# Kernel optimization log

Hardware: AMD Instinct MI355X
Metric: run time of the kernel (lower is better)

The kernel has to match this reference:

```python
import jax, jax.numpy as jnp
import numpy as np

B, DIM, W0, H0 = 4, 256, 128, 128
HEADS, HEAD_DIM = 8, 32
FOLD, PROP = 2, 4
EPS_GN = 1e-5


def _l2norm(x):
    n = jnp.linalg.norm(x, axis=-1, keepdims=True)
    return x / jnp.maximum(n, 1e-12)  # matches F.normalize eps


def _fold(t, f):
    # (b, c, f*w, f*h) -> (b*f*f, c, w, h), matching einops '(b f1 f2)' ordering
    b, c, W, H = t.shape
    w, h = W // f, H // f
    return t.reshape(b, c, f, w, f, h).transpose(0, 2, 4, 1, 3, 5).reshape(b * f * f, c, w, h)


def _unfold(t, f, b0):
    bf, c, w, h = t.shape
    return t.reshape(b0, f, f, c, w, h).transpose(0, 3, 1, 4, 2, 5).reshape(b0, c, f * w, f * h)


def _pool(t, p):
    # AdaptiveAvgPool2d((p, p)) for divisible sizes
    b, c, w, h = t.shape
    return t.reshape(b, c, p, w // p, p, h // p).mean(axis=(3, 5))


def setup_inputs() -> dict:
    key = jax.random.key(0)
    ks = jax.random.split(key, 6)
    D = HEADS * HEAD_DIM
    return {
        "x": jax.random.normal(ks[0], (B, DIM, W0, H0), jnp.float32),
        "xyz": jax.random.normal(ks[1], (B, 3, W0, H0), jnp.float32),
        "Wv": jax.random.normal(ks[2], (D, DIM, 7, 7), jnp.float32) * 0.02,
        "bv": jnp.zeros((D,), jnp.float32),
        "Wproj": jax.random.normal(ks[3], (DIM, D), jnp.float32) * 0.02,
        "bproj": jnp.zeros((DIM,), jnp.float32),
        "gn_w": jnp.ones((D,), jnp.float32),
        "gn_b": jnp.zeros((D,), jnp.float32),
        "sim_alpha": jnp.ones((1,), jnp.float32),
        "sim_beta": jnp.zeros((1,), jnp.float32),
    }


def reference(x, xyz, Wv, bv, Wproj, bproj, gn_w, gn_b, sim_alpha, sim_beta):
    # value = self.v(x): 7x7 conv, padding 3
    value = jax.lax.conv_general_dilated(
        x, Wv, (1, 1), ((3, 3), (3, 3)),
        dimension_numbers=("NCHW", "OIHW", "NCHW")) + bv[None, :, None, None]
    b0 = x.shape[0]
    # heads split: 'b (e c) w h -> (b e) c w h'
    xh = x.reshape(b0 * HEADS, HEAD_DIM, W0, H0)
    vh = value.reshape(b0 * HEADS, HEAD_DIM, W0, H0)
    xf = _fold(xh, FOLD)
    vf = _fold(vh, FOLD)
    xyzf = _fold(xyz, FOLD)
    bb, c, w, h = xf.shape
    M = PROP * PROP
    N = w * h
    centers = _pool(xf, PROP)                                   # (bb, c, p, p)
    xyz_c = _pool(xyzf, PROP)
    value_centers = _pool(vf, PROP).reshape(bb, c, M).transpose(0, 2, 1)  # (bb, M, c)
    cen = centers.reshape(bb, c, M).transpose(0, 2, 1)          # (bb, M, c)
    xpts = xf.reshape(bb, c, N).transpose(0, 2, 1)              # (bb, N, c)
    vpts = vf.reshape(bb, c, N).transpose(0, 2, 1)              # (bb, N, c)
    sim = jax.nn.sigmoid(sim_beta + sim_alpha *
                         jnp.einsum('bmc,bnc->bmn', _l2norm(cen), _l2norm(xpts)))
    bg = xyzf.shape[0]
    xyz_pts = xyzf.reshape(bg, 3, N).transpose(0, 2, 1)
    xyz_cc = xyz_c.reshape(bg, 3, M).transpose(0, 2, 1)
    sim_geo = jax.nn.sigmoid(sim_beta + sim_alpha *
                             jnp.einsum('bmc,bnc->bmn', _l2norm(xyz_cc), _l2norm(xyz_pts)))
    sim_geo = jnp.tile(sim_geo, (sim.shape[0] // sim_geo.shape[0], 1, 1))  # torch .repeat
    sim = sim * sim_geo ** 2
    # faithful mask math: scatter_(1, argmax, 1.0) into an all-ones tensor leaves it all-ones,
    # so dense_mask == 1 and split_mask == 0 exactly as in the source.
    dense_mask = jnp.ones_like(sim)
    split_mask = 1.0 - dense_mask
    denss_sim = sim * dense_mask
    split_sim = sim * split_mask
    split_out = (jnp.einsum('bmn,bnc->bmc', split_sim, vpts) + value_centers) \
                / (split_sim.sum(-1, keepdims=True) + 1.0)
    denss_out = (jnp.einsum('bmn,bnc->bmc', denss_sim, xpts) + cen) \
                / (denss_sim.sum(-1, keepdims=True) + 1.0)
    denss_pts = jnp.einsum('bmc,bmn->bnc', denss_out, denss_sim)  # (bb, N, c)
    split_pts = jnp.einsum('bmc,bmn->bnc', split_out, split_sim)
    out = (denss_pts + split_pts).transpose(0, 2, 1).reshape(bb, c, w, h)
    out = _unfold(out, FOLD, b0 * HEADS)
    out = out.reshape(b0, HEADS * HEAD_DIM, W0, H0)
    # GroupNorm with 1 group: normalize over (C, H, W) per sample
    mu = out.mean(axis=(1, 2, 3), keepdims=True)
    var = ((out - mu) ** 2).mean(axis=(1, 2, 3), keepdims=True)
    out = (out - mu) / jnp.sqrt(var + EPS_GN)
    out = out * gn_w[None, :, None, None] + gn_b[None, :, None, None]
    # proj 1x1 conv + silu
    out = jnp.einsum('bchw,oc->bohw', out, Wproj) + bproj[None, :, None, None]
    return jax.nn.silu(out)
```

## Files before the change

### kernel.cpp

```cpp
#include <hip/hip_runtime.h>
#include <stdint.h>


typedef __attribute__((ext_vector_type(8))) short short8;
typedef __attribute__((ext_vector_type(4))) float floatx4;
typedef _Float16 half8 __attribute__((ext_vector_type(8)));

#define XS_STRIDE 264
#define SIM_STRIDE 264

__device__ float g_sbp[2048*2];
__device__ float g_alpha[1024];
__device__ float g_bias[1024];
__device__ unsigned short g_Wbf[65536];
__device__ float g_cenraw[128*16*32];
__device__ float g_cenhat[128*16*32];
__device__ float g_gcenhat[16*16*4];
__device__ __attribute__((aligned(16))) _Float16 g_sim[(size_t)128*4096*16];
__device__ float g_dnum[128*16*16*32];
__device__ float g_rsum[128*16*16];

static __device__ __forceinline__ unsigned short f2bu(float f) {
  unsigned u = __float_as_uint(f);
  u += 0x7fffu + ((u >> 16) & 1u);
  return (unsigned short)(u >> 16);
}
static __device__ __forceinline__ float sum16(const float* p) {
  const float4* q = (const float4*)p;
  float4 a = q[0], b = q[1], c = q[2], d = q[3];
  return (a.x+a.y+a.z+a.w) + (b.x+b.y+b.z+b.w) + (c.x+c.y+c.z+c.w) + (d.x+d.y+d.z+d.w);
}

__global__ __launch_bounds__(64) void k0_geo(const float* __restrict__ xyz) {
  __shared__ float gc[64];
  const int gti = blockIdx.x;
  const int bg = gti >> 2, f1 = (gti >> 1) & 1, f2 = gti & 1;
  const int t = threadIdx.x;
  if (t < 48) {
    const int m = t / 3, ch = t - 3*(t/3);
    const int pi = m >> 2, pj = m & 3;
    const float* p = xyz + (size_t)(bg*3+ch)*16384 + (f1*64 + pi*16)*128 + f2*64 + pj*16;
    float s = 0.f;
    #pragma unroll
    for (int r = 0; r < 16; ++r) s += sum16(p + r*128);
    gc[m*4+ch] = s * (1.f/256.f);
  }
  __syncthreads();
  if (t < 16) {
    float g0 = gc[t*4], g1 = gc[t*4+1], g2 = gc[t*4+2];
    float inv = 1.f / fmaxf(sqrtf(g0*g0+g1*g1+g2*g2), 1e-12f);
    float* o = g_gcenhat + gti*64 + t*4;
    o[0] = g0*inv; o[1] = g1*inv; o[2] = g2*inv; o[3] = 0.f;
  }
}

__global__ __launch_bounds__(128) void k1a_cen(const float* __restrict__ x) {
  __shared__ float cenL[128];
  __shared__ float invL[4];
  const int blk = blockIdx.x;
  const int bb = blk >> 2, pi = blk & 3;
  const int b = bb >> 5, e = (bb >> 2) & 7, f1 = (bb >> 1) & 1, f2 = bb & 1;
  const int tid = threadIdx.x;
  const int c = tid >> 2, pj = tid & 3;
  const int m = pi*4 + pj;
  const float* p = x + ((size_t)(b*256 + e*32 + c)*128 + f1*64 + pi*16)*128 + f2*64 + pj*16;
  float s = 0.f;
  #pragma unroll
  for (int r = 0; r < 16; ++r) s += sum16(p + r*128);
  const float raw = s * (1.f/256.f);
  cenL[pj*32 + c] = raw;
  g_cenraw[(bb*16 + m)*32 + c] = raw;
  __syncthreads();
  if (tid < 4) {
    float ss = 0.f;
    #pragma unroll
    for (int cc = 0; cc < 32; ++cc) { float v = cenL[tid*32+cc]; ss += v*v; }
    invL[tid] = 1.f / fmaxf(sqrtf(ss), 1e-12f);
  }
  __syncthreads();
  g_cenhat[(bb*16 + m)*32 + c] = raw * invL[pj];
}

__global__ __launch_bounds__(256) void k1b_sim(const float* __restrict__ x,
                                               const float* __restrict__ xyz,
                                               const float* __restrict__ salpha,
                                               const float* __restrict__ sbeta) {
  __shared__ float xs[32*XS_STRIDE];
  __shared__ _Float16 simL[16*SIM_STRIDE];
  __shared__ float cenhatL[512];
  __shared__ float gcenL[64];
  __shared__ float rsW[4*16];
  const int blk = blockIdx.x;
  const int bb = blk >> 4, ck = blk & 15;
  const int b = bb >> 5, e = (bb >> 2) & 7, f1 = (bb >> 1) & 1, f2 = bb & 1;
  const int gti = ((e & 3) << 2) | (f1 << 1) | f2;
  const int tid = threadIdx.x, lane = tid & 63, wave = tid >> 6;
  const float alpha = salpha[0], beta = sbeta[0];
  const float* xt = x + (((size_t)(b*256 + e*32))*128 + f1*64)*128 + f2*64;

  cenhatL[tid]       = g_cenhat[bb*512 + tid];
  cenhatL[tid + 256] = g_cenhat[bb*512 + tid + 256];
  if (tid < 64) gcenL[tid] = g_gcenhat[gti*64 + tid];
  {
    const int c = tid >> 3, q = tid & 7;
    const float* src = xt + (size_t)c*16384 + (ck*4)*128;
    float* dst = xs + c*XS_STRIDE;
    #pragma unroll
    for (int k = 0; k < 8; ++k) {
      const int j = q + k*8;
      const int lr = j >> 4, lc = (j & 15)*4;
      *(float4*)(dst + lr*64 + lc) = *(const float4*)(src + lr*128 + lc);
    }
  }
  const int ng = ck*256 + tid;
  const int wi = ng >> 6, hi = ng & 63;
  float g0, g1, g2;
  {
    const float* gp = xyz + (size_t)((e & 3)*3)*16384 + (f1*64 + wi)*128 + f2*64 + hi;
    g0 = gp[0]; g1 = gp[16384]; g2 = gp[32768];
    float invg = 1.f / fmaxf(sqrtf(g0*g0+g1*g1+g2*g2), 1e-12f);
    g0 *= invg; g1 *= invg; g2 *= invg;
  }
  __syncthreads();

  float xn[32]; float ss = 0.f;
  #pragma unroll
  for (int c2 = 0; c2 < 32; ++c2) { float v = xs[c2*XS_STRIDE + tid]; xn[c2] = v; ss += v*v; }
  const float invn = 1.f / fmaxf(sqrtf(ss), 1e-12f);
  _Float16 sv[16];
  #pragma unroll
  for (int m = 0; m < 16; ++m) {
    const float* chp = cenhatL + m*32;
    float d = 0.f;
    #pragma unroll
    for (int c2 = 0; c2 < 32; ++c2) d += chp[c2]*xn[c2];
    d *= invn;
    const float* gh = gcenL + m*4;
    const float dg = gh[0]*g0 + gh[1]*g1 + gh[2]*g2;
    const float s  = 1.f/(1.f + __expf(-(beta + alpha*d)));
    const float gg = 1.f/(1.f + __expf(-(beta + alpha*dg)));
    const _Float16 h = (_Float16)(s*gg*gg);
    sv[m] = h;
    simL[m*SIM_STRIDE + tid] = h;
  }
  {
    half8 p0, p1;
    #pragma unroll
    for (int m = 0; m < 8; ++m) { p0[m] = sv[m]; p1[m] = sv[8+m]; }
    _Float16* gp = g_sim + ((size_t)bb*4096 + ng)*16;
    *(half8*)gp = p0;
    *(half8*)(gp + 8) = p1;
  }
  #pragma unroll
  for (int m = 0; m < 16; ++m) {
    float v = (float)sv[m];
    #pragma unroll
    for (int off = 1; off < 64; off <<= 1) v += __shfl_xor(v, off, 64);
    if (lane == 0) rsW[wave*16 + m] = v;
  }
  __syncthreads();
  if (tid < 16) g_rsum[(bb*16 + ck)*16 + tid] = rsW[tid] + rsW[16+tid] + rsW[32+tid] + rsW[48+tid];

  #pragma unroll
  for (int t2 = 0; t2 < 2; ++t2) {
    const int task = tid + t2*256;
    const int m = task & 15, c2 = task >> 4;
    const _Float16* sp = simL + m*SIM_STRIDE;
    const float* xp = xs + c2*XS_STRIDE;
    float acc = 0.f;
    #pragma unroll 4
    for (int j = 0; j < 32; ++j) {
      const half8 sh = *(const half8*)(sp + j*8);
      const float4 xa = *(const float4*)(xp + j*8);
      const float4 xb = *(const float4*)(xp + j*8 + 4);
      acc += (float)sh[0]*xa.x + (float)sh[1]*xa.y + (float)sh[2]*xa.z + (float)sh[3]*xa.w
           + (float)sh[4]*xb.x + (float)sh[5]*xb.y + (float)sh[6]*xb.z + (float)sh[7]*xb.w;
    }
    g_dnum[(((size_t)bb*16 + ck)*16 + m)*32 + c2] = acc;
  }
}

__global__ __launch_bounds__(256) void k1d_out(float* __restrict__ outv) {
  __shared__ float denssL[512];
  __shared__ float rsL[16];
  __shared__ float sred[8];
  const int blk = blockIdx.x;
  const int bb = blk >> 4, ck = blk & 15;
  const int b = bb >> 5, e = (bb >> 2) & 7, f1 = (bb >> 1) & 1, f2 = bb & 1;
  const int tid = threadIdx.x, lane = tid & 63, wave = tid >> 6;
  if (tid < 16) {
    float r = 1.f;
    #pragma unroll
    for (int k2 = 0; k2 < 16; ++k2) r += g_rsum[(bb*16 + k2)*16 + tid];
    rsL[tid] = r;
  }
  __syncthreads();
  #pragma unroll
  for (int t2 = 0; t2 < 2; ++t2) {
    const int idx = tid + t2*256;
    const int m = idx >> 5, c = idx & 31;
    float a = g_cenraw[bb*512 + idx];
    #pragma unroll
    for (int k2 = 0; k2 < 16; ++k2) a += g_dnum[(((size_t)bb*16 + k2)*16 + m)*32 + c];
    denssL[idx] = a / rsL[m];
  }
  __syncthreads();
  const int ng = ck*256 + tid;
  const int wi = ng >> 6, hi = ng & 63;
  float sarr[16];
  {
    const _Float16* gp = g_sim + ((size_t)bb*4096 + ng)*16;
    const half8 p0 = *(const half8*)gp;
    const half8 p1 = *(const half8*)(gp + 8);
    #pragma unroll
    for (int m = 0; m < 8; ++m) { sarr[m] = (float)p0[m]; sarr[8+m] = (float)p1[m]; }
  }
  float o[32];
  #pragma unroll
  for (int c = 0; c < 32; ++c) o[c] = 0.f;
  #pragma unroll
  for (int m = 0; m < 16; ++m) {
    const float s = sarr[m];
    const float* dp = denssL + m*32;
    #pragma unroll
    for (int c = 0; c < 32; ++c) o[c] += s*dp[c];
  }
  float* ob = outv + (((size_t)(b*256 + e*32))*128 + f1*64)*128 + f2*64 + wi*128 + hi;
  float s1 = 0.f, s2 = 0.f;
  #pragma unroll
  for (int c = 0; c < 32; ++c) { const float v = o[c]; s1 += v; s2 += v*v; ob[(size_t)c*16384] = v; }
  #pragma unroll
  for (int off = 1; off < 64; off <<= 1) { s1 += __shfl_xor(s1, off, 64); s2 += __shfl_xor(s2, off, 64); }
  if (lane == 0) { sred[wave] = s1; sred[4+wave] = s2; }
  __syncthreads();
  if (tid == 0) {
    g_sbp[blk*2]   = sred[0]+sred[1]+sred[2]+sred[3];
    g_sbp[blk*2+1] = sred[4]+sred[5]+sred[6]+sred[7];
  }
}

__global__ __launch_bounds__(256) void k2_prep(const float* __restrict__ Wp,
                                               const float* __restrict__ bpr,
                                               const float* __restrict__ gnw,
                                               const float* __restrict__ gnb) {
  __shared__ float betaL[256];
  __shared__ float rr[8];
  const int b = blockIdx.x, t = threadIdx.x, lane = t & 63, wave = t >> 6;
  float s1 = g_sbp[(b*512 + t)*2]     + g_sbp[(b*512 + 256 + t)*2];
  float s2 = g_sbp[(b*512 + t)*2 + 1] + g_sbp[(b*512 + 256 + t)*2 + 1];
  #pragma unroll
  for (int off = 1; off < 64; off <<= 1) { s1 += __shfl_xor(s1, off, 64); s2 += __shfl_xor(s2, off, 64); }
  if (lane == 0) { rr[wave] = s1; rr[4+wave] = s2; }
  __syncthreads();
  const float S1 = rr[0]+rr[1]+rr[2]+rr[3];
  const float S2 = rr[4]+rr[5]+rr[6]+rr[7];
  const float inv_n = 1.f / 4194304.f;
  const float mu  = S1 * inv_n;
  const float inv = rsqrtf(fmaxf(S2*inv_n - mu*mu, 0.f) + 1e-5f);
  const float a = inv * gnw[t];
  g_alpha[b*256 + t] = a;
  betaL[t] = gnb[t] - mu * a;
  __syncthreads();
  float k = bpr[t];
  const float* wr = Wp + t*256;
  for (int c = 0; c < 256; c += 4) {
    const float4 w = *(const float4*)(wr + c);
    k += w.x*betaL[c+0] + w.y*betaL[c+1] + w.z*betaL[c+2] + w.w*betaL[c+3];
  }
  g_bias[b*256 + t] = k;
  const int base = (b*256 + t)*64;
  for (int i = 0; i < 64; i += 4) {
    const float4 w = *(const float4*)(Wp + base + i);
    g_Wbf[base+i+0] = f2bu(w.x); g_Wbf[base+i+1] = f2bu(w.y);
    g_Wbf[base+i+2] = f2bu(w.z); g_Wbf[base+i+3] = f2bu(w.w);
  }
}

__global__ __launch_bounds__(256) void k3_proj(float* __restrict__ v) {
  __shared__ unsigned short vt[64*264];
  __shared__ float alphaL[256];
  __shared__ float biasL[256];
  const int blk = blockIdx.x;
  const int b = blk >> 8;
  const int p0 = (blk & 255) * 64;
  const int tid = threadIdx.x;
  alphaL[tid] = g_alpha[b*256 + tid];
  biasL[tid]  = g_bias[b*256 + tid];
  __syncthreads();
  {
    const int oct = tid >> 5, cl = tid & 31;
    #pragma unroll
    for (int i = 0; i < 8; ++i) {
      const int c = cl + 32*i;
      const float* src = v + ((size_t)(b*256 + c))*16384 + p0 + oct*8;
      const float4 r0 = *(const float4*)(src);
      const float4 r1 = *(const float4*)(src + 4);
      const float a = alphaL[c];
      unsigned short* w = vt + (oct*8)*264 + c;
      w[0*264] = f2bu(r0.x*a); w[1*264] = f2bu(r0.y*a);
      w[2*264] = f2bu(r0.z*a); w[3*264] = f2bu(r0.w*a);
      w[4*264] = f2bu(r1.x*a); w[5*264] = f2bu(r1.y*a);
      w[6*264] = f2bu(r1.z*a); w[7*264] = f2bu(r1.w*a);
    }
  }
  __syncthreads();
  const int lane = tid & 63, wave = tid >> 6;
  const int lm = lane & 15, quad = lane >> 4;
  const int m0 = wave*64;
  floatx4 acc[4][4] = {};
  #pragma unroll
  for (int ks = 0; ks < 8; ++ks) {
    const int k0 = ks*32 + quad*8;
    short8 afr[4], bfr[4];
    #pragma unroll
    for (int mi = 0; mi < 4; ++mi)
      afr[mi] = *(const short8*)((const short*)g_Wbf + (size_t)(m0 + mi*16 + lm)*256 + k0);
    #pragma unroll
    for (int ni = 0; ni < 4; ++ni)
      bfr[ni] = *(const short8*)((const short*)vt + (ni*16 + lm)*264 + k0);
    #pragma unroll
    for (int mi = 0; mi < 4; ++mi) {
      #pragma unroll
      for (int ni = 0; ni < 4; ++ni)
        acc[mi][ni] = __builtin_amdgcn_mfma_f32_16x16x32_bf16(afr[mi], bfr[ni], acc[mi][ni], 0, 0, 0);
    }
  }
  #pragma unroll
  for (int mi = 0; mi < 4; ++mi) {
    #pragma unroll
    for (int r = 0; r < 4; ++r) {
      const int o = m0 + mi*16 + quad*4 + r;
      const float kb = biasL[o];
      #pragma unroll
      for (int ni = 0; ni < 4; ++ni) {
        float val = acc[mi][ni][r] + kb;
        val = val / (1.f + __expf(-val));
        v[((size_t)(b*256 + o))*16384 + p0 + ni*16 + lm] = val;
      }
    }
  }
}

extern "C" void kernel_launch(void* const* d_in, const int* in_sizes, int n_in,
                              void* d_out, int out_size, void* d_ws, size_t ws_size,
                              hipStream_t stream)
{
  (void)in_sizes; (void)n_in; (void)d_ws; (void)ws_size; (void)out_size;
  const float* x     = (const float*)d_in[0];
  const float* xyz   = (const float*)d_in[1];
  const float* Wproj = (const float*)d_in[4];
  const float* bproj = (const float*)d_in[5];
  const float* gnw   = (const float*)d_in[6];
  const float* gnb   = (const float*)d_in[7];
  const float* sa    = (const float*)d_in[8];
  const float* sb    = (const float*)d_in[9];
  float* out = (float*)d_out;

  hipLaunchKernelGGL(k0_geo,  dim3(16),   dim3(64),  0, stream, xyz);
  hipLaunchKernelGGL(k1a_cen, dim3(512),  dim3(128), 0, stream, x);
  hipLaunchKernelGGL(k1b_sim, dim3(2048), dim3(256), 0, stream, x, xyz, sa, sb);
  hipLaunchKernelGGL(k1d_out, dim3(2048), dim3(256), 0, stream, out);
  hipLaunchKernelGGL(k2_prep, dim3(4),    dim3(256), 0, stream, Wproj, bproj, gnw, gnb);
  hipLaunchKernelGGL(k3_proj, dim3(1024), dim3(256), 0, stream, out);
}
```

Measured before the change: 269.1 us.

## Stage pre-norm output in fp16 layout, fold GN scale into weights, split reductions

The intermediate attention output is now written as an fp16 point-major buffer instead of fp32 NCHW into the output tensor. The projection GEMM reads it directly as fp16 MFMA operands, with the GroupNorm scale folded into per-batch fp16 weights, so the LDS transpose and conversion stage is gone. The dense-center reduction moves to a new small kernel so it is no longer recomputed by every block of k1d_out. Similarity and output dot products switch to packed fp16 fdot2, and the sim kernel drops its x LDS staging in favour of direct global loads. This cuts memory traffic and redundant work but adds fp16 precision loss and one more launch.

```diff
diff --git a/kernel.cpp b/kernel.cpp
--- a/kernel.cpp
+++ b/kernel.cpp
@@ -4,31 +4,43 @@
 
 typedef __attribute__((ext_vector_type(8))) short short8;
 typedef __attribute__((ext_vector_type(4))) float floatx4;
-typedef _Float16 half8 __attribute__((ext_vector_type(8)));
-
-#define XS_STRIDE 264
-#define SIM_STRIDE 264
+typedef __fp16 fp16x2 __attribute__((ext_vector_type(2)));
+
+#define SIMS_DW 260
 
 __device__ float g_sbp[2048*2];
 __device__ float g_alpha[1024];
 __device__ float g_bias[1024];
-__device__ unsigned short g_Wbf[65536];
+__device__ __attribute__((aligned(16))) _Float16 g_Wa[4*256*256];
 __device__ float g_cenraw[128*16*32];
 __device__ float g_cenhat[128*16*32];
 __device__ float g_gcenhat[16*16*4];
 __device__ __attribute__((aligned(16))) _Float16 g_sim[(size_t)128*4096*16];
 __device__ float g_dnum[128*16*16*32];
 __device__ float g_rsum[128*16*16];
-
-static __device__ __forceinline__ unsigned short f2bu(float f) {
-  unsigned u = __float_as_uint(f);
-  u += 0x7fffu + ((u >> 16) & 1u);
-  return (unsigned short)(u >> 16);
-}
+__device__ unsigned g_dnh2[128*256];
+__device__ __attribute__((aligned(16))) _Float16 g_preout[(size_t)128*4096*32];
+
+static __device__ __forceinline__ fp16x2 as_h2(unsigned u) { return __builtin_bit_cast(fp16x2, u); }
+static __device__ __forceinline__ unsigned pk(float a, float b) {
+  return __builtin_bit_cast(unsigned, __builtin_amdgcn_cvt_pkrtz(a, b));
+}
+#if __has_builtin(__builtin_amdgcn_fdot2)
+static __device__ __forceinline__ float fdot2(fp16x2 a, fp16x2 b, float c) {
+  return __builtin_amdgcn_fdot2(a, b, c, false);
+}
+#else
+static __device__ __forceinline__ float fdot2(fp16x2 a, fp16x2 b, float c) {
+  return c + (float)a[0]*(float)b[0] + (float)a[1]*(float)b[1];
+}
+#endif
 static __device__ __forceinline__ float sum16(const float* p) {
   const float4* q = (const float4*)p;
   float4 a = q[0], b = q[1], c = q[2], d = q[3];
   return (a.x+a.y+a.z+a.w) + (b.x+b.y+b.z+b.w) + (c.x+c.y+c.z+c.w) + (d.x+d.y+d.z+d.w);
+}
+static __device__ __forceinline__ float sigm(float z) {
+  return __builtin_amdgcn_rcpf(1.f + __expf(-z));
 }
 
 __global__ __launch_bounds__(64) void k0_geo(const float* __restrict__ xyz) {
@@ -81,15 +93,14 @@
   g_cenhat[(bb*16 + m)*32 + c] = raw * invL[pj];
 }
 
-__global__ __launch_bounds__(256) void k1b_sim(const float* __restrict__ x,
-                                               const float* __restrict__ xyz,
-                                               const float* __restrict__ salpha,
-                                               const float* __restrict__ sbeta) {
-  __shared__ float xs[32*XS_STRIDE];
-  __shared__ _Float16 simL[16*SIM_STRIDE];
-  __shared__ float cenhatL[512];
+__global__ __launch_bounds__(256, 4) void k1b_sim(const float* __restrict__ x,
+                                                  const float* __restrict__ xyz,
+                                                  const float* __restrict__ salpha,
+                                                  const float* __restrict__ sbeta) {
+  __shared__ float simS[16*SIMS_DW];
+  __shared__ unsigned chP[256];
   __shared__ float gcenL[64];
-  __shared__ float rsW[4*16];
+  __shared__ float rsW[64];
   const int blk = blockIdx.x;
   const int bb = blk >> 4, ck = blk & 15;
   const int b = bb >> 5, e = (bb >> 2) & 7, f1 = (bb >> 1) & 1, f2 = bb & 1;
@@ -98,62 +109,58 @@
   const float alpha = salpha[0], beta = sbeta[0];
   const float* xt = x + (((size_t)(b*256 + e*32))*128 + f1*64)*128 + f2*64;
 
-  cenhatL[tid]       = g_cenhat[bb*512 + tid];
-  cenhatL[tid + 256] = g_cenhat[bb*512 + tid + 256];
+  {
+    const float2 cp = *(const float2*)(g_cenhat + bb*512 + tid*2);
+    chP[tid] = pk(cp.x, cp.y);
+  }
   if (tid < 64) gcenL[tid] = g_gcenhat[gti*64 + tid];
-  {
-    const int c = tid >> 3, q = tid & 7;
-    const float* src = xt + (size_t)c*16384 + (ck*4)*128;
-    float* dst = xs + c*XS_STRIDE;
-    #pragma unroll
-    for (int k = 0; k < 8; ++k) {
-      const int j = q + k*8;
-      const int lr = j >> 4, lc = (j & 15)*4;
-      *(float4*)(dst + lr*64 + lc) = *(const float4*)(src + lr*128 + lc);
-    }
-  }
+  __syncthreads();
+
   const int ng = ck*256 + tid;
   const int wi = ng >> 6, hi = ng & 63;
+  const int addr = wi*128 + hi;
+  float xn[32]; float ss = 0.f;
+  #pragma unroll
+  for (int c = 0; c < 32; ++c) { float v = xt[(size_t)c*16384 + addr]; xn[c] = v; ss += v*v; }
+  unsigned xp[16];
+  #pragma unroll
+  for (int p = 0; p < 16; ++p) xp[p] = pk(xn[2*p], xn[2*p+1]);
+  const float invn = __builtin_amdgcn_rcpf(fmaxf(sqrtf(ss), 1e-12f));
   float g0, g1, g2;
   {
     const float* gp = xyz + (size_t)((e & 3)*3)*16384 + (f1*64 + wi)*128 + f2*64 + hi;
     g0 = gp[0]; g1 = gp[16384]; g2 = gp[32768];
-    float invg = 1.f / fmaxf(sqrtf(g0*g0+g1*g1+g2*g2), 1e-12f);
+    float invg = __builtin_amdgcn_rcpf(fmaxf(sqrtf(g0*g0+g1*g1+g2*g2), 1e-12f));
     g0 *= invg; g1 *= invg; g2 *= invg;
   }
-  __syncthreads();
-
-  float xn[32]; float ss = 0.f;
-  #pragma unroll
-  for (int c2 = 0; c2 < 32; ++c2) { float v = xs[c2*XS_STRIDE + tid]; xn[c2] = v; ss += v*v; }
-  const float invn = 1.f / fmaxf(sqrtf(ss), 1e-12f);
-  _Float16 sv[16];
+  float svf[16];
   #pragma unroll
   for (int m = 0; m < 16; ++m) {
-    const float* chp = cenhatL + m*32;
     float d = 0.f;
     #pragma unroll
-    for (int c2 = 0; c2 < 32; ++c2) d += chp[c2]*xn[c2];
+    for (int p = 0; p < 16; ++p) d = fdot2(as_h2(chP[m*16+p]), as_h2(xp[p]), d);
     d *= invn;
     const float* gh = gcenL + m*4;
     const float dg = gh[0]*g0 + gh[1]*g1 + gh[2]*g2;
-    const float s  = 1.f/(1.f + __expf(-(beta + alpha*d)));
-    const float gg = 1.f/(1.f + __expf(-(beta + alpha*dg)));
-    const _Float16 h = (_Float16)(s*gg*gg);
-    sv[m] = h;
-    simL[m*SIM_STRIDE + tid] = h;
-  }
-  {
-    half8 p0, p1;
-    #pragma unroll
-    for (int m = 0; m < 8; ++m) { p0[m] = sv[m]; p1[m] = sv[8+m]; }
+    const float s  = sigm(beta + alpha*d);
+    const float gg = sigm(beta + alpha*dg);
+    const float sv = s*gg*gg;
+    svf[m] = sv;
+    simS[m*SIMS_DW + tid] = sv;
+  }
+  {
+    uint4 o0, o1;
+    o0.x = pk(svf[0],svf[1]);   o0.y = pk(svf[2],svf[3]);
+    o0.z = pk(svf[4],svf[5]);   o0.w = pk(svf[6],svf[7]);
+    o1.x = pk(svf[8],svf[9]);   o1.y = pk(svf[10],svf[11]);
+    o1.z = pk(svf[12],svf[13]); o1.w = pk(svf[14],svf[15]);
     _Float16* gp = g_sim + ((size_t)bb*4096 + ng)*16;
-    *(half8*)gp = p0;
-    *(half8*)(gp + 8) = p1;
+    *(uint4*)gp = o0;
+    *(uint4*)(gp + 8) = o1;
   }
   #pragma unroll
   for (int m = 0; m < 16; ++m) {
-    float v = (float)sv[m];
+    float v = svf[m];
     #pragma unroll
     for (int off = 1; off < 64; off <<= 1) v += __shfl_xor(v, off, 64);
     if (lane == 0) rsW[wave*16 + m] = v;
@@ -164,71 +171,84 @@
   #pragma unroll
   for (int t2 = 0; t2 < 2; ++t2) {
     const int task = tid + t2*256;
-    const int m = task & 15, c2 = task >> 4;
-    const _Float16* sp = simL + m*SIM_STRIDE;
-    const float* xp = xs + c2*XS_STRIDE;
+    const int m = task & 15, c = task >> 4;
+    const float* sp = simS + m*SIMS_DW;
+    const float* px = xt + (size_t)c*16384 + ck*512;
     float acc = 0.f;
-    #pragma unroll 4
+    #pragma unroll 2
     for (int j = 0; j < 32; ++j) {
-      const half8 sh = *(const half8*)(sp + j*8);
-      const float4 xa = *(const float4*)(xp + j*8);
-      const float4 xb = *(const float4*)(xp + j*8 + 4);
-      acc += (float)sh[0]*xa.x + (float)sh[1]*xa.y + (float)sh[2]*xa.z + (float)sh[3]*xa.w
-           + (float)sh[4]*xb.x + (float)sh[5]*xb.y + (float)sh[6]*xb.z + (float)sh[7]*xb.w;
+      const int a0 = (j >> 3)*128 + (j & 7)*8;
+      const float4 xa = *(const float4*)(px + a0);
+      const float4 xb = *(const float4*)(px + a0 + 4);
+      const float4 sa = *(const float4*)(sp + j*8);
+      const float4 sb = *(const float4*)(sp + j*8 + 4);
+      acc += sa.x*xa.x + sa.y*xa.y + sa.z*xa.z + sa.w*xa.w
+           + sb.x*xb.x + sb.y*xb.y + sb.z*xb.z + sb.w*xb.w;
     }
-    g_dnum[(((size_t)bb*16 + ck)*16 + m)*32 + c2] = acc;
-  }
-}
-
-__global__ __launch_bounds__(256) void k1d_out(float* __restrict__ outv) {
+    g_dnum[(((size_t)bb*16 + ck)*16 + m)*32 + c] = acc;
+  }
+}
+
+__global__ __launch_bounds__(512) void k1c_red() {
   __shared__ float denssL[512];
   __shared__ float rsL[16];
+  const int bb = blockIdx.x, tid = threadIdx.x;
+  if (tid < 16) {
+    float r = 1.f;
+    #pragma unroll
+    for (int k = 0; k < 16; ++k) r += g_rsum[(bb*16 + k)*16 + tid];
+    rsL[tid] = r;
+  }
+  float a = g_cenraw[bb*512 + tid];
+  #pragma unroll
+  for (int k = 0; k < 16; ++k) a += g_dnum[(size_t)bb*8192 + k*512 + tid];
+  __syncthreads();
+  denssL[tid] = a / rsL[tid >> 5];
+  __syncthreads();
+  if (tid < 256) {
+    const int c = tid >> 3, mp = tid & 7;
+    g_dnh2[bb*256 + c*8 + mp] = pk(denssL[(2*mp)*32 + c], denssL[(2*mp+1)*32 + c]);
+  }
+}
+
+__global__ __launch_bounds__(256, 4) void k1d_out() {
+  __shared__ unsigned dl[256];
   __shared__ float sred[8];
   const int blk = blockIdx.x;
   const int bb = blk >> 4, ck = blk & 15;
-  const int b = bb >> 5, e = (bb >> 2) & 7, f1 = (bb >> 1) & 1, f2 = bb & 1;
   const int tid = threadIdx.x, lane = tid & 63, wave = tid >> 6;
-  if (tid < 16) {
-    float r = 1.f;
-    #pragma unroll
-    for (int k2 = 0; k2 < 16; ++k2) r += g_rsum[(bb*16 + k2)*16 + tid];
-    rsL[tid] = r;
-  }
-  __syncthreads();
-  #pragma unroll
-  for (int t2 = 0; t2 < 2; ++t2) {
-    const int idx = tid + t2*256;
-    const int m = idx >> 5, c = idx & 31;
-    float a = g_cenraw[bb*512 + idx];
-    #pragma unroll
-    for (int k2 = 0; k2 < 16; ++k2) a += g_dnum[(((size_t)bb*16 + k2)*16 + m)*32 + c];
-    denssL[idx] = a / rsL[m];
-  }
+  dl[tid] = g_dnh2[bb*256 + tid];
   __syncthreads();
   const int ng = ck*256 + tid;
-  const int wi = ng >> 6, hi = ng & 63;
-  float sarr[16];
+  unsigned sp[8];
   {
     const _Float16* gp = g_sim + ((size_t)bb*4096 + ng)*16;
-    const half8 p0 = *(const half8*)gp;
-    const half8 p1 = *(const half8*)(gp + 8);
-    #pragma unroll
-    for (int m = 0; m < 8; ++m) { sarr[m] = (float)p0[m]; sarr[8+m] = (float)p1[m]; }
-  }
-  float o[32];
-  #pragma unroll
-  for (int c = 0; c < 32; ++c) o[c] = 0.f;
-  #pragma unroll
-  for (int m = 0; m < 16; ++m) {
-    const float s = sarr[m];
-    const float* dp = denssL + m*32;
-    #pragma unroll
-    for (int c = 0; c < 32; ++c) o[c] += s*dp[c];
-  }
-  float* ob = outv + (((size_t)(b*256 + e*32))*128 + f1*64)*128 + f2*64 + wi*128 + hi;
+    const uint4 q0 = *(const uint4*)gp;
+    const uint4 q1 = *(const uint4*)(gp + 8);
+    sp[0]=q0.x; sp[1]=q0.y; sp[2]=q0.z; sp[3]=q0.w;
+    sp[4]=q1.x; sp[5]=q1.y; sp[6]=q1.z; sp[7]=q1.w;
+  }
+  float out[32];
+  #pragma unroll
+  for (int c = 0; c < 32; ++c) {
+    float acc = 0.f;
+    #pragma unroll
+    for (int mp = 0; mp < 8; ++mp) acc = fdot2(as_h2(sp[mp]), as_h2(dl[c*8 + mp]), acc);
+    out[c] = acc;
+  }
   float s1 = 0.f, s2 = 0.f;
   #pragma unroll
-  for (int c = 0; c < 32; ++c) { const float v = o[c]; s1 += v; s2 += v*v; ob[(size_t)c*16384] = v; }
+  for (int c = 0; c < 32; ++c) { s1 += out[c]; s2 += out[c]*out[c]; }
+  {
+    uint4 w[4];
+    #pragma unroll
+    for (int q = 0; q < 4; ++q) {
+      w[q].x = pk(out[8*q+0], out[8*q+1]); w[q].y = pk(out[8*q+2], out[8*q+3]);
+      w[q].z = pk(out[8*q+4], out[8*q+5]); w[q].w = pk(out[8*q+6], out[8*q+7]);
+    }
+    _Float16* gp = g_preout + ((size_t)bb*4096 + ng)*32;
+    *(uint4*)gp = w[0]; *(uint4*)(gp+8) = w[1]; *(uint4*)(gp+16) = w[2]; *(uint4*)(gp+24) = w[3];
+  }
   #pragma unroll
   for (int off = 1; off < 64; off <<= 1) { s1 += __shfl_xor(s1, off, 64); s2 += __shfl_xor(s2, off, 64); }
   if (lane == 0) { sred[wave] = s1; sred[4+wave] = s2; }
@@ -244,6 +264,7 @@
                                                const float* __restrict__ gnw,
                                                const float* __restrict__ gnb) {
   __shared__ float betaL[256];
+  __shared__ float alphaL[256];
   __shared__ float rr[8];
   const int b = blockIdx.x, t = threadIdx.x, lane = t & 63, wave = t >> 6;
   float s1 = g_sbp[(b*512 + t)*2]     + g_sbp[(b*512 + 256 + t)*2];
@@ -259,70 +280,56 @@
   const float inv = rsqrtf(fmaxf(S2*inv_n - mu*mu, 0.f) + 1e-5f);
   const float a = inv * gnw[t];
   g_alpha[b*256 + t] = a;
+  alphaL[t] = a;
   betaL[t] = gnb[t] - mu * a;
   __syncthreads();
   float k = bpr[t];
   const float* wr = Wp + t*256;
-  for (int c = 0; c < 256; c += 4) {
-    const float4 w = *(const float4*)(wr + c);
-    k += w.x*betaL[c+0] + w.y*betaL[c+1] + w.z*betaL[c+2] + w.w*betaL[c+3];
+  _Float16* wa = g_Wa + ((size_t)b*256 + t)*256;
+  for (int c = 0; c < 256; c += 8) {
+    const float4 w0 = *(const float4*)(wr + c);
+    const float4 w1 = *(const float4*)(wr + c + 4);
+    k += w0.x*betaL[c+0] + w0.y*betaL[c+1] + w0.z*betaL[c+2] + w0.w*betaL[c+3]
+       + w1.x*betaL[c+4] + w1.y*betaL[c+5] + w1.z*betaL[c+6] + w1.w*betaL[c+7];
+    uint4 o;
+    o.x = pk(w0.x*alphaL[c+0], w0.y*alphaL[c+1]);
+    o.y = pk(w0.z*alphaL[c+2], w0.w*alphaL[c+3]);
+    o.z = pk(w1.x*alphaL[c+4], w1.y*alphaL[c+5]);
+    o.w = pk(w1.z*alphaL[c+6], w1.w*alphaL[c+7]);
+    *(uint4*)(wa + c) = o;
   }
   g_bias[b*256 + t] = k;
-  const int base = (b*256 + t)*64;
-  for (int i = 0; i < 64; i += 4) {
-    const float4 w = *(const float4*)(Wp + base + i);
-    g_Wbf[base+i+0] = f2bu(w.x); g_Wbf[base+i+1] = f2bu(w.y);
-    g_Wbf[base+i+2] = f2bu(w.z); g_Wbf[base+i+3] = f2bu(w.w);
-  }
-}
-
-__global__ __launch_bounds__(256) void k3_proj(float* __restrict__ v) {
-  __shared__ unsigned short vt[64*264];
-  __shared__ float alphaL[256];
+}
+
+__global__ __launch_bounds__(256, 4) void k3_proj(float* __restrict__ out) {
   __shared__ float biasL[256];
   const int blk = blockIdx.x;
-  const int b = blk >> 8;
-  const int p0 = (blk & 255) * 64;
-  const int tid = threadIdx.x;
-  alphaL[tid] = g_alpha[b*256 + tid];
-  biasL[tid]  = g_bias[b*256 + tid];
-  __syncthreads();
-  {
-    const int oct = tid >> 5, cl = tid & 31;
-    #pragma unroll
-    for (int i = 0; i < 8; ++i) {
-      const int c = cl + 32*i;
-      const float* src = v + ((size_t)(b*256 + c))*16384 + p0 + oct*8;
-      const float4 r0 = *(const float4*)(src);
-      const float4 r1 = *(const float4*)(src + 4);
-      const float a = alphaL[c];
-      unsigned short* w = vt + (oct*8)*264 + c;
-      w[0*264] = f2bu(r0.x*a); w[1*264] = f2bu(r0.y*a);
-      w[2*264] = f2bu(r0.z*a); w[3*264] = f2bu(r0.w*a);
-      w[4*264] = f2bu(r1.x*a); w[5*264] = f2bu(r1.y*a);
-      w[6*264] = f2bu(r1.z*a); w[7*264] = f2bu(r1.w*a);
-    }
-  }
-  __syncthreads();
-  const int lane = tid & 63, wave = tid >> 6;
+  const int b = blk >> 8, pb = blk & 255;
+  const int f1 = pb >> 7, f2 = pb & 1;
+  const int nbase = ((pb >> 1) & 63) * 64;
+  const int tid = threadIdx.x, lane = tid & 63, wave = tid >> 6;
   const int lm = lane & 15, quad = lane >> 4;
   const int m0 = wave*64;
+  biasL[tid] = g_bias[b*256 + tid];
+  __syncthreads();
   floatx4 acc[4][4] = {};
   #pragma unroll
   for (int ks = 0; ks < 8; ++ks) {
-    const int k0 = ks*32 + quad*8;
+    const _Float16* bbase = g_preout
+        + ((size_t)(b*32 + ks*4 + f1*2 + f2)*4096 + nbase)*32 + quad*8;
+    const _Float16* abase = g_Wa + ((size_t)b*256)*256 + (size_t)ks*32 + quad*8;
     short8 afr[4], bfr[4];
     #pragma unroll
     for (int mi = 0; mi < 4; ++mi)
-      afr[mi] = *(const short8*)((const short*)g_Wbf + (size_t)(m0 + mi*16 + lm)*256 + k0);
+      afr[mi] = *(const short8*)(abase + (size_t)(m0 + mi*16 + lm)*256);
     #pragma unroll
     for (int ni = 0; ni < 4; ++ni)
-      bfr[ni] = *(const short8*)((const short*)vt + (ni*16 + lm)*264 + k0);
+      bfr[ni] = *(const short8*)(bbase + (ni*16 + lm)*32);
     #pragma unroll
     for (int mi = 0; mi < 4; ++mi) {
       #pragma unroll
       for (int ni = 0; ni < 4; ++ni)
-        acc[mi][ni] = __builtin_amdgcn_mfma_f32_16x16x32_bf16(afr[mi], bfr[ni], acc[mi][ni], 0, 0, 0);
+        acc[mi][ni] = __builtin_amdgcn_mfma_f32_16x16x32_f16(afr[mi], bfr[ni], acc[mi][ni], 0, 0, 0);
     }
   }
   #pragma unroll
@@ -334,8 +341,8 @@
       #pragma unroll
       for (int ni = 0; ni < 4; ++ni) {
         float val = acc[mi][ni][r] + kb;
-        val = val / (1.f + __expf(-val));
-        v[((size_t)(b*256 + o))*16384 + p0 + ni*16 + lm] = val;
+        val = val * sigm(val);
+        out[((size_t)(b*256 + o))*16384 + pb*64 + ni*16 + lm] = val;
       }
     }
   }
@@ -359,7 +366,8 @@
   hipLaunchKernelGGL(k0_geo,  dim3(16),   dim3(64),  0, stream, xyz);
   hipLaunchKernelGGL(k1a_cen, dim3(512),  dim3(128), 0, stream, x);
   hipLaunchKernelGGL(k1b_sim, dim3(2048), dim3(256), 0, stream, x, xyz, sa, sb);
-  hipLaunchKernelGGL(k1d_out, dim3(2048), dim3(256), 0, stream, out);
+  hipLaunchKernelGGL(k1c_red, dim3(128),  dim3(512), 0, stream);
+  hipLaunchKernelGGL(k1d_out, dim3(2048), dim3(256), 0, stream);
   hipLaunchKernelGGL(k2_prep, dim3(4),    dim3(256), 0, stream, Wproj, bproj, gnw, gnb);
   hipLaunchKernelGGL(k3_proj, dim3(1024), dim3(256), 0, stream, out);
 }
```

After: 268.7 us. About the same (-0.2%).
